# Optimization experiments

Hardware: AMD Instinct MI355X
Metric: run time of the kernel (lower is better)

## Reference

```python
import jax, jax.numpy as jnp
import numpy as np

N = 100000
E = 3200000
G = 2000
EPS = 1e-5

def gcn_conv(x, W, b, src, dst):
    # PyG GCNConv: add self-loops, symmetric deg^-1/2 normalization,
    # out_i = sum_j norm_ij * (x_j @ W) + b
    loop = jnp.arange(N, dtype=src.dtype)
    s = jnp.concatenate([src, loop])
    d = jnp.concatenate([dst, loop])
    deg = jax.ops.segment_sum(jnp.ones_like(d, dtype=x.dtype), d, num_segments=N)
    dinv = jax.lax.rsqrt(jnp.maximum(deg, 1.0))
    norm = dinv[s] * dinv[d]                      # [E+N]
    h = x @ W                                     # [N, out]
    msg = h[s] * norm[:, None]                    # gather + scale
    return jax.ops.segment_sum(msg, d, num_segments=N) + b

def batchnorm(h, g, be):
    mu = jnp.mean(h, axis=0)
    var = jnp.mean((h - mu) ** 2, axis=0)
    return (h - mu) * jax.lax.rsqrt(var + EPS) * g + be

def setup_inputs() -> dict:
    key = jax.random.key(0)
    ks = jax.random.split(key, 16)
    inp = {
        "x": jax.random.normal(ks[0], (N, 10), dtype=jnp.float32),
        "src": jax.random.randint(ks[1], (E,), 0, N, dtype=jnp.int32),
        "dst": jax.random.randint(ks[2], (E,), 0, N, dtype=jnp.int32),
        "batch": jnp.sort(jax.random.randint(ks[3], (N,), 0, G, dtype=jnp.int32)),
        "W1": jax.random.normal(ks[4], (10, 64), dtype=jnp.float32) * 0.3,
        "b1": jnp.zeros((64,), jnp.float32),
        "g1": jnp.ones((64,), jnp.float32),
        "be1": jnp.zeros((64,), jnp.float32),
        "W2": jax.random.normal(ks[5], (64, 128), dtype=jnp.float32) * 0.12,
        "b2": jnp.zeros((128,), jnp.float32),
        "g2": jnp.ones((128,), jnp.float32),
        "be2": jnp.zeros((128,), jnp.float32),
        "fW1": jax.random.normal(ks[6], (128, 64), dtype=jnp.float32) * 0.09,
        "fb1": jnp.zeros((64,), jnp.float32),
        "fW2": jax.random.normal(ks[7], (64, 1), dtype=jnp.float32) * 0.12,
        "fb2": jnp.zeros((1,), jnp.float32),
    }
    return inp

def reference(x, src, dst, batch, W1, b1, g1, be1, W2, b2, g2, be2, fW1, fb1, fW2, fb2):
    h = jax.nn.relu(batchnorm(gcn_conv(x, W1, b1, src, dst), g1, be1))
    h = jax.nn.relu(batchnorm(gcn_conv(h, W2, b2, src, dst), g2, be2))
    # global_mean_pool over graphs
    s = jax.ops.segment_sum(h, batch, num_segments=G)
    cnt = jax.ops.segment_sum(jnp.ones((N,), h.dtype), batch, num_segments=G)
    pooled = s / jnp.maximum(cnt, 1.0)[:, None]   # [G, 128]
    # dropout is identity in eval mode
    h = jax.nn.relu(pooled @ fW1 + fb1)
    return h @ fW2 + fb2                          # [G, 1]
```

## Files before the change

kernel.cpp:

```cpp
#include <hip/hip_runtime.h>
#include <hip/hip_fp16.h>

#define NN 100000
#define NE 3200000
#define NG 2000
#define NB 391
#define BKT_SH 8
#define EPB 4096
#define PAD 16
#define CAP 10240
static constexpr float BN_EPS = 1e-5f;

typedef _Float16 f16x8 __attribute__((ext_vector_type(8)));
typedef float    f32x4 __attribute__((ext_vector_type(4)));

__global__ __launch_bounds__(1024) void k_init(int* bcur, float* s1, float* s2) {
    int t = threadIdx.x;
    if (t < NB) bcur[t * PAD] = t * CAP;
    if (t < 128) s1[t] = 0.f;
    if (t < 256) s2[t] = 0.f;
}

__global__ __launch_bounds__(256) void k_bucket(const int* __restrict__ src, const int* __restrict__ dst,
                                                int* __restrict__ bcur, int* __restrict__ stage) {
    __shared__ int cnt[NB];
    __shared__ int base[NB];
    int t = threadIdx.x;
    long long e0 = (long long)blockIdx.x * EPB;
    int ew[EPB / 256], eb[EPB / 256];
#pragma unroll
    for (int i = 0; i < EPB / 256; ++i) {
        long long e = e0 + t + i * 256;
        if (e < NE) {
            int d = dst[e];
            ew[i] = ((d & 255) << 17) | src[e];
            eb[i] = d >> BKT_SH;
        } else eb[i] = -1;
    }
    for (int i = t; i < NB; i += 256) cnt[i] = 0;
    __syncthreads();
#pragma unroll
    for (int i = 0; i < EPB / 256; ++i)
        if (eb[i] >= 0) atomicAdd(&cnt[eb[i]], 1);
    __syncthreads();
    for (int i = t; i < NB; i += 256) {
        int c = cnt[i];
        base[i] = c ? atomicAdd(&bcur[i * PAD], c) : 0;
    }
    __syncthreads();
    for (int i = t; i < NB; i += 256) cnt[i] = 0;
    __syncthreads();
#pragma unroll
    for (int i = 0; i < EPB / 256; ++i) {
        if (eb[i] >= 0) {
            int pos = base[eb[i]] + atomicAdd(&cnt[eb[i]], 1);
            stage[pos] = ew[i];
        }
    }
}

__global__ __launch_bounds__(256) void k_csr(const int* __restrict__ stage,
                                             const int* __restrict__ bcur, const float* __restrict__ x,
                                             int* __restrict__ deg_i, int* __restrict__ row_start,
                                             float* __restrict__ dinv, int* __restrict__ srcs,
                                             __half2* __restrict__ xh2) {
    __shared__ int ldeg[256];
    __shared__ int scn[256];
    __shared__ int lcur[256];
    int t = threadIdx.x;
    int b = blockIdx.x;
    int base = b * CAP;
    int end  = bcur[b * PAD];
    ldeg[t] = 0;
    __syncthreads();
    for (int e = base + t; e < end; e += 256)
        atomicAdd(&ldeg[(stage[e] >> 17) & 255], 1);
    __syncthreads();
    int v = ldeg[t];
    scn[t] = v;
    __syncthreads();
#pragma unroll
    for (int off = 1; off < 256; off <<= 1) {
        int a = (t >= off) ? scn[t - off] : 0;
        __syncthreads();
        scn[t] += a;
        __syncthreads();
    }
    int rs = base + scn[t] - v;
    lcur[t] = rs;
    int i = (b << BKT_SH) + t;
    if (i < NN) {
        deg_i[i] = v;
        row_start[i] = rs;
        float dv = rsqrtf((float)(v + 1));
        dinv[i] = dv;
        float xv[10];
#pragma unroll
        for (int k = 0; k < 10; ++k) xv[k] = x[i * 10 + k] * dv;
#pragma unroll
        for (int c = 0; c < 8; ++c) {
            float a = (2 * c < 10) ? xv[2 * c] : 0.f;
            float bb = (2 * c + 1 < 10) ? xv[2 * c + 1] : 0.f;
            xh2[i * 8 + c] = __floats2half2_rn(a, bb);
        }
    }
    __syncthreads();
    for (int e = base + t; e < end; e += 256) {
        int w = stage[e];
        int pos = atomicAdd(&lcur[(w >> 17) & 255], 1);
        srcs[pos] = w & 0x1FFFF;
    }
}

__global__ __launch_bounds__(256) void k_gather1(const float4* __restrict__ xh4, const int* __restrict__ srcs,
                                                 const int* __restrict__ row_start, const int* __restrict__ deg,
                                                 const float* __restrict__ dinv, float4* __restrict__ aggx4) {
    int lane = threadIdx.x & 63;
    int wid  = threadIdx.x >> 6;
    int d = blockIdx.x * 4 + wid;
    if (d >= NN) return;
    int c = lane & 1;
    int g = lane >> 1;
    int start = row_start[d];
    int cnt   = deg[d];
    float acc[8] = {0.f};
    for (int k = g; k < cnt; k += 32) {
        int s = srcs[start + k];
        float4 r = xh4[s * 2 + c];
        const __half2* p = (const __half2*)&r;
#pragma unroll
        for (int j = 0; j < 4; ++j) {
            float2 u = __half22float2(p[j]);
            acc[2 * j] += u.x; acc[2 * j + 1] += u.y;
        }
    }
    if (g == 0) {
        float4 r = xh4[d * 2 + c];
        const __half2* p = (const __half2*)&r;
#pragma unroll
        for (int j = 0; j < 4; ++j) {
            float2 u = __half22float2(p[j]);
            acc[2 * j] += u.x; acc[2 * j + 1] += u.y;
        }
    }
#pragma unroll
    for (int m = 2; m < 64; m <<= 1) {
#pragma unroll
        for (int j = 0; j < 8; ++j) acc[j] += __shfl_xor(acc[j], m, 64);
    }
    if (g == 0) {
        float dd = dinv[d];
        float4 o0 = make_float4(dd * acc[0], dd * acc[1], dd * acc[2], dd * acc[3]);
        float4 o1 = make_float4(dd * acc[4], dd * acc[5], dd * acc[6], dd * acc[7]);
        aggx4[d * 4 + c * 2]     = o0;
        aggx4[d * 4 + c * 2 + 1] = o1;
    }
}

__global__ __launch_bounds__(256) void k_mm1s(const float* __restrict__ aggx, const float* __restrict__ W,
                                              const float* __restrict__ b, __half* __restrict__ h1h,
                                              float* __restrict__ sums1) {
    __shared__ float ls[256];
    __shared__ float lq[256];
    int t = threadIdx.x;
    int rg = t >> 6;
    int f = t & 63;
    float w[10];
#pragma unroll
    for (int k = 0; k < 10; ++k) w[k] = W[k * 64 + f];
    float bf = b[f];
    float s = 0.f, q = 0.f;
    for (int row = blockIdx.x * 4 + rg; row < NN; row += 512 * 4) {
        float acc = bf;
#pragma unroll
        for (int k = 0; k < 10; ++k) acc += aggx[row * 16 + k] * w[k];
        s += acc; q += acc * acc;
        h1h[row * 64 + f] = __float2half(acc);
    }
    ls[t] = s; lq[t] = q;
    __syncthreads();
    if (t < 64) {
        float S = ls[t] + ls[t + 64] + ls[t + 128] + ls[t + 192];
        float Q = lq[t] + lq[t + 64] + lq[t + 128] + lq[t + 192];
        atomicAdd(&sums1[f], S);
        atomicAdd(&sums1[64 + f], Q);
    }
}

__global__ __launch_bounds__(256) void k_bn_apply1h(const float4* __restrict__ h1h4, const float* __restrict__ sums1,
                                                    const float* __restrict__ g, const float* __restrict__ be,
                                                    const float* __restrict__ dinv, int2* __restrict__ h1f8) {
    int idx = blockIdx.x * 256 + threadIdx.x;
    if (idx >= NN * 8) return;
    int i = idx >> 3;
    int c = idx & 7;
    const float invn = 1.0f / (float)NN;
    float dv = dinv[i];
    float4 r = h1h4[idx];
    const __half2* p = (const __half2*)&r;
    float rv[8];
#pragma unroll
    for (int j = 0; j < 4; ++j) {
        int f0 = 8 * c + 2 * j, f1 = f0 + 1;
        float mu0 = sums1[f0] * invn, mu1 = sums1[f1] * invn;
        float sc0 = g[f0] * rsqrtf(sums1[64 + f0] * invn - mu0 * mu0 + BN_EPS);
        float sc1 = g[f1] * rsqrtf(sums1[64 + f1] * invn - mu1 * mu1 + BN_EPS);
        float2 u = __half22float2(p[j]);
        rv[2 * j]     = fmaxf((u.x - mu0) * sc0 + be[f0], 0.f) * dv;
        rv[2 * j + 1] = fmaxf((u.y - mu1) * sc1 + be[f1], 0.f) * dv;
    }
    int lo = __builtin_amdgcn_cvt_pk_fp8_f32(rv[0], rv[1], 0, false);
    lo     = __builtin_amdgcn_cvt_pk_fp8_f32(rv[2], rv[3], lo, true);
    int hi = __builtin_amdgcn_cvt_pk_fp8_f32(rv[4], rv[5], 0, false);
    hi     = __builtin_amdgcn_cvt_pk_fp8_f32(rv[6], rv[7], hi, true);
    h1f8[idx] = make_int2(lo, hi);
}

__global__ __launch_bounds__(256) void k_gather2(const int4* __restrict__ h16, const int* __restrict__ srcs,
                                                 const int* __restrict__ row_start, const int* __restrict__ deg,
                                                 const float* __restrict__ dinv, float4* __restrict__ aggh4) {
    int lane = threadIdx.x & 63;
    int wid  = threadIdx.x >> 6;
    int d = blockIdx.x * 4 + wid;
    if (d >= NN) return;
    int c = lane & 3;
    int g = lane >> 2;
    int start = row_start[d];
    int cnt   = deg[d];
    float acc[16];
#pragma unroll
    for (int j = 0; j < 16; ++j) acc[j] = 0.f;
    for (int k = g; k < cnt; k += 16) {
        int s = srcs[start + k];
        int4 w = h16[(long long)s * 4 + c];
#pragma unroll
        for (int j = 0; j < 4; ++j) {
            int wi = (&w.x)[j];
            auto lo = __builtin_amdgcn_cvt_pk_f32_fp8(wi, false);
            auto hi = __builtin_amdgcn_cvt_pk_f32_fp8(wi, true);
            acc[4 * j]     += lo[0]; acc[4 * j + 1] += lo[1];
            acc[4 * j + 2] += hi[0]; acc[4 * j + 3] += hi[1];
        }
    }
    if (g == 0) {
        int4 w = h16[(long long)d * 4 + c];
#pragma unroll
        for (int j = 0; j < 4; ++j) {
            int wi = (&w.x)[j];
            auto lo = __builtin_amdgcn_cvt_pk_f32_fp8(wi, false);
            auto hi = __builtin_amdgcn_cvt_pk_f32_fp8(wi, true);
            acc[4 * j]     += lo[0]; acc[4 * j + 1] += lo[1];
            acc[4 * j + 2] += hi[0]; acc[4 * j + 3] += hi[1];
        }
    }
#pragma unroll
    for (int m = 4; m < 64; m <<= 1) {
#pragma unroll
        for (int j = 0; j < 16; ++j) acc[j] += __shfl_xor(acc[j], m, 64);
    }
    if (g == 0) {
        float dd = dinv[d];
        __half2 o[8];
#pragma unroll
        for (int j = 0; j < 8; ++j)
            o[j] = __floats2half2_rn(dd * acc[2 * j], dd * acc[2 * j + 1]);
        const float4* of = (const float4*)o;
        aggh4[d * 8 + c * 2]     = of[0];
        aggh4[d * 8 + c * 2 + 1] = of[1];
    }
}

__global__ __launch_bounds__(256) void k_mm2m(const __half* __restrict__ aggh, const float* __restrict__ W,
                                              const float* __restrict__ b, __half* __restrict__ h2,
                                              float* __restrict__ sums2) {
    int t = threadIdx.x;
    __shared__ _Float16 w2h[64 * 128];
    for (int i = t; i < 64 * 128; i += 256) w2h[i] = (_Float16)W[i];
    __syncthreads();

    int lane = t & 63;
    int wid  = t >> 6;
    int quad = lane >> 4;
    int n16  = lane & 15;

    f16x8 bfr[8][2];
#pragma unroll
    for (int nt = 0; nt < 8; ++nt)
#pragma unroll
        for (int kk = 0; kk < 2; ++kk)
#pragma unroll
            for (int j = 0; j < 8; ++j)
                bfr[nt][kk][j] = w2h[(kk * 32 + quad * 8 + j) * 128 + nt * 16 + n16];
    float bcol[8];
#pragma unroll
    for (int nt = 0; nt < 8; ++nt) bcol[nt] = b[nt * 16 + n16];

    const f16x8* a8 = (const f16x8*)aggh;
    float s[8] = {0.f}, q[8] = {0.f};

    for (int rt = blockIdx.x * 4 + wid; rt < NN / 16; rt += 256 * 4) {
        int arow = rt * 16 + n16;
        f16x8 a0 = a8[arow * 8 + quad];
        f16x8 a1 = a8[arow * 8 + 4 + quad];
#pragma unroll
        for (int nt = 0; nt < 8; ++nt) {
            f32x4 c = {0.f, 0.f, 0.f, 0.f};
            c = __builtin_amdgcn_mfma_f32_16x16x32_f16(a0, bfr[nt][0], c, 0, 0, 0);
            c = __builtin_amdgcn_mfma_f32_16x16x32_f16(a1, bfr[nt][1], c, 0, 0, 0);
            float bb = bcol[nt];
#pragma unroll
            for (int reg = 0; reg < 4; ++reg) {
                float v = c[reg] + bb;
                s[nt] += v; q[nt] += v * v;
                int row = rt * 16 + quad * 4 + reg;
                h2[(long long)row * 128 + nt * 16 + n16] = __float2half(v);
            }
        }
    }
#pragma unroll
    for (int nt = 0; nt < 8; ++nt) {
        s[nt] += __shfl_xor(s[nt], 16, 64); s[nt] += __shfl_xor(s[nt], 32, 64);
        q[nt] += __shfl_xor(q[nt], 16, 64); q[nt] += __shfl_xor(q[nt], 32, 64);
    }
    __shared__ float lsS[4][128];
    __shared__ float lsQ[4][128];
    if (lane < 16) {
#pragma unroll
        for (int nt = 0; nt < 8; ++nt) {
            lsS[wid][nt * 16 + lane] = s[nt];
            lsQ[wid][nt * 16 + lane] = q[nt];
        }
    }
    __syncthreads();
    if (t < 128) {
        float S = lsS[0][t] + lsS[1][t] + lsS[2][t] + lsS[3][t];
        float Q = lsQ[0][t] + lsQ[1][t] + lsQ[2][t] + lsQ[3][t];
        atomicAdd(&sums2[t], S);
        atomicAdd(&sums2[128 + t], Q);
    }
}

__global__ __launch_bounds__(128) void k_pool(const __half* __restrict__ h2, const float* __restrict__ sums2,
                                              const float* __restrict__ g, const float* __restrict__ be,
                                              const int* __restrict__ batch, float* __restrict__ pooled) {
    int gb = blockIdx.x;
    int f = threadIdx.x;
    int lo = 0, hi = NN;
    while (lo < hi) { int mid = (lo + hi) >> 1; if (batch[mid] < gb) lo = mid + 1; else hi = mid; }
    int start = lo;
    hi = NN;
    while (lo < hi) { int mid = (lo + hi) >> 1; if (batch[mid] < gb + 1) lo = mid + 1; else hi = mid; }
    int end = lo;

    const float invn = 1.0f / (float)NN;
    float mu = sums2[f] * invn;
    float sc = g[f] * rsqrtf(sums2[128 + f] * invn - mu * mu + BN_EPS);
    float bb = be[f];
    float acc = 0.f;
    for (int i = start; i < end; ++i) {
        float v = __half2float(h2[(long long)i * 128 + f]);
        acc += fmaxf((v - mu) * sc + bb, 0.f);
    }
    float inv = 1.0f / fmaxf((float)(end - start), 1.0f);
    pooled[gb * 128 + f] = acc * inv;
}

__global__ __launch_bounds__(64) void k_mlp(const float* __restrict__ pooled,
                                            const float* __restrict__ fW1, const float* __restrict__ fb1,
                                            const float* __restrict__ fW2, const float* __restrict__ fb2,
                                            float* __restrict__ out) {
    int g = blockIdx.x;
    int j = threadIdx.x;
    float acc = fb1[j];
#pragma unroll
    for (int k = 0; k < 128; ++k) acc += pooled[g * 128 + k] * fW1[k * 64 + j];
    float hj = fmaxf(acc, 0.f) * fW2[j];
#pragma unroll
    for (int off = 32; off > 0; off >>= 1) hj += __shfl_down(hj, off, 64);
    if (j == 0) out[g] = hj + fb2[0];
}

extern "C" void kernel_launch(void* const* d_in, const int* in_sizes, int n_in,
                              void* d_out, int out_size, void* d_ws, size_t ws_size,
                              hipStream_t stream) {
    const float* x    = (const float*)d_in[0];
    const int*   src  = (const int*)d_in[1];
    const int*   dst  = (const int*)d_in[2];
    const int*   batch= (const int*)d_in[3];
    const float* W1   = (const float*)d_in[4];
    const float* b1   = (const float*)d_in[5];
    const float* g1   = (const float*)d_in[6];
    const float* be1  = (const float*)d_in[7];
    const float* W2   = (const float*)d_in[8];
    const float* b2   = (const float*)d_in[9];
    const float* g2   = (const float*)d_in[10];
    const float* be2  = (const float*)d_in[11];
    const float* fW1  = (const float*)d_in[12];
    const float* fb1  = (const float*)d_in[13];
    const float* fW2  = (const float*)d_in[14];
    const float* fb2  = (const float*)d_in[15];
    float* out = (float*)d_out;

    float* ws        = (float*)d_ws;
    int*   deg_i     = (int*)ws;
    int*   row_start = deg_i + NN;
    float* dinv      = (float*)(row_start + NN);
    int*   bcur      = (int*)(dinv + NN);
    float* sums1     = (float*)(bcur + NB * PAD);
    float* sums2     = sums1 + 128;
    float* h1R       = sums2 + 256;
    float* agghR     = h1R + NN * 64;
    float* h2R       = agghR + NN * 64;
    __half2* xh2     = (__half2*)h1R;
    __half*  h1h     = (__half*)h1R;
    float*   pooled  = h1R;
    int*     stage   = (int*)agghR;
    __half*  aggh    = (__half*)agghR;
    float*   aggx    = h2R;
    int*     srcs    = (int*)(h2R + NN * 16);
    int2*    h1f8    = (int2*)(h2R + NN * 16 + NB * CAP);
    __half*  h2      = (__half*)h2R;

    k_init<<<1, 1024, 0, stream>>>(bcur, sums1, sums2);
    k_bucket<<<(NE + EPB - 1) / EPB, 256, 0, stream>>>(src, dst, bcur, stage);
    k_csr<<<NB, 256, 0, stream>>>(stage, bcur, x, deg_i, row_start, dinv, srcs, xh2);

    k_gather1<<<(NN + 3) / 4, 256, 0, stream>>>((const float4*)xh2, srcs, row_start, deg_i, dinv, (float4*)aggx);
    k_mm1s<<<512, 256, 0, stream>>>(aggx, W1, b1, h1h, sums1);
    k_bn_apply1h<<<(NN * 8 + 255) / 256, 256, 0, stream>>>((const float4*)h1h, sums1, g1, be1, dinv, h1f8);

    k_gather2<<<(NN + 3) / 4, 256, 0, stream>>>((const int4*)h1f8, srcs, row_start, deg_i, dinv, (float4*)aggh);
    k_mm2m<<<256, 256, 0, stream>>>(aggh, W2, b2, h2, sums2);

    k_pool<<<NG, 128, 0, stream>>>(h2, sums2, g2, be2, batch, pooled);
    k_mlp<<<NG, 64, 0, stream>>>(pooled, fW1, fb1, fW2, fb2, out);
}
```

Measured before the change: 375.8 us.

## Remap gather kernels to lane-per-feature-chunk with multiple nodes per wavefront

Both neighbor-aggregation kernels change from one wavefront per destination node, with lanes split across edges and a cross-lane shuffle reduction, to several nodes per wavefront. Each lane owns a small feature slice and walks that node's whole edge list serially, unrolled by two. This removes the shuffle reductions and the idle lanes left when a node has fewer edges than lane groups, with an average degree of about 32. In exchange, the gather loads per lane are narrower (4 bytes instead of 16) and each lane runs a longer serial dependency chain over edges.

```diff
diff --git a/kernel.cpp b/kernel.cpp
--- a/kernel.cpp
+++ b/kernel.cpp
@@ -112,49 +112,37 @@
     }
 }
 
-__global__ __launch_bounds__(256) void k_gather1(const float4* __restrict__ xh4, const int* __restrict__ srcs,
+__global__ __launch_bounds__(256) void k_gather1(const __half2* __restrict__ xh2, const int* __restrict__ srcs,
                                                  const int* __restrict__ row_start, const int* __restrict__ deg,
-                                                 const float* __restrict__ dinv, float4* __restrict__ aggx4) {
+                                                 const float* __restrict__ dinv, float2* __restrict__ aggx2) {
     int lane = threadIdx.x & 63;
     int wid  = threadIdx.x >> 6;
-    int d = blockIdx.x * 4 + wid;
+    int sub  = lane >> 3;
+    int li   = lane & 7;
+    int d = blockIdx.x * 32 + wid * 8 + sub;
     if (d >= NN) return;
-    int c = lane & 1;
-    int g = lane >> 1;
     int start = row_start[d];
     int cnt   = deg[d];
-    float acc[8] = {0.f};
-    for (int k = g; k < cnt; k += 32) {
+    float ax = 0.f, ay = 0.f;
+    int k = 0;
+    for (; k + 2 <= cnt; k += 2) {
+        int s0 = srcs[start + k];
+        int s1 = srcs[start + k + 1];
+        float2 u0 = __half22float2(xh2[s0 * 8 + li]);
+        float2 u1 = __half22float2(xh2[s1 * 8 + li]);
+        ax += u0.x + u1.x; ay += u0.y + u1.y;
+    }
+    if (k < cnt) {
         int s = srcs[start + k];
-        float4 r = xh4[s * 2 + c];
-        const __half2* p = (const __half2*)&r;
-#pragma unroll
-        for (int j = 0; j < 4; ++j) {
-            float2 u = __half22float2(p[j]);
-            acc[2 * j] += u.x; acc[2 * j + 1] += u.y;
-        }
-    }
-    if (g == 0) {
-        float4 r = xh4[d * 2 + c];
-        const __half2* p = (const __half2*)&r;
-#pragma unroll
-        for (int j = 0; j < 4; ++j) {
-            float2 u = __half22float2(p[j]);
-            acc[2 * j] += u.x; acc[2 * j + 1] += u.y;
-        }
-    }
-#pragma unroll
-    for (int m = 2; m < 64; m <<= 1) {
-#pragma unroll
-        for (int j = 0; j < 8; ++j) acc[j] += __shfl_xor(acc[j], m, 64);
-    }
-    if (g == 0) {
-        float dd = dinv[d];
-        float4 o0 = make_float4(dd * acc[0], dd * acc[1], dd * acc[2], dd * acc[3]);
-        float4 o1 = make_float4(dd * acc[4], dd * acc[5], dd * acc[6], dd * acc[7]);
-        aggx4[d * 4 + c * 2]     = o0;
-        aggx4[d * 4 + c * 2 + 1] = o1;
-    }
+        float2 u = __half22float2(xh2[s * 8 + li]);
+        ax += u.x; ay += u.y;
+    }
+    {
+        float2 u = __half22float2(xh2[d * 8 + li]);
+        ax += u.x; ay += u.y;
+    }
+    float dd = dinv[d];
+    aggx2[d * 8 + li] = make_float2(dd * ax, dd * ay);
 }
 
 __global__ __launch_bounds__(256) void k_mm1s(const float* __restrict__ aggx, const float* __restrict__ W,
@@ -216,58 +204,48 @@
     h1f8[idx] = make_int2(lo, hi);
 }
 
-__global__ __launch_bounds__(256) void k_gather2(const int4* __restrict__ h16, const int* __restrict__ srcs,
+__global__ __launch_bounds__(256) void k_gather2(const int* __restrict__ h1f8i, const int* __restrict__ srcs,
                                                  const int* __restrict__ row_start, const int* __restrict__ deg,
-                                                 const float* __restrict__ dinv, float4* __restrict__ aggh4) {
+                                                 const float* __restrict__ dinv, float2* __restrict__ aggh2) {
     int lane = threadIdx.x & 63;
     int wid  = threadIdx.x >> 6;
-    int d = blockIdx.x * 4 + wid;
+    int sub  = lane >> 4;
+    int li   = lane & 15;
+    int d = blockIdx.x * 16 + wid * 4 + sub;
     if (d >= NN) return;
-    int c = lane & 3;
-    int g = lane >> 2;
     int start = row_start[d];
     int cnt   = deg[d];
-    float acc[16];
-#pragma unroll
-    for (int j = 0; j < 16; ++j) acc[j] = 0.f;
-    for (int k = g; k < cnt; k += 16) {
-        int s = srcs[start + k];
-        int4 w = h16[(long long)s * 4 + c];
-#pragma unroll
-        for (int j = 0; j < 4; ++j) {
-            int wi = (&w.x)[j];
-            auto lo = __builtin_amdgcn_cvt_pk_f32_fp8(wi, false);
-            auto hi = __builtin_amdgcn_cvt_pk_f32_fp8(wi, true);
-            acc[4 * j]     += lo[0]; acc[4 * j + 1] += lo[1];
-            acc[4 * j + 2] += hi[0]; acc[4 * j + 3] += hi[1];
-        }
-    }
-    if (g == 0) {
-        int4 w = h16[(long long)d * 4 + c];
-#pragma unroll
-        for (int j = 0; j < 4; ++j) {
-            int wi = (&w.x)[j];
-            auto lo = __builtin_amdgcn_cvt_pk_f32_fp8(wi, false);
-            auto hi = __builtin_amdgcn_cvt_pk_f32_fp8(wi, true);
-            acc[4 * j]     += lo[0]; acc[4 * j + 1] += lo[1];
-            acc[4 * j + 2] += hi[0]; acc[4 * j + 3] += hi[1];
-        }
-    }
-#pragma unroll
-    for (int m = 4; m < 64; m <<= 1) {
-#pragma unroll
-        for (int j = 0; j < 16; ++j) acc[j] += __shfl_xor(acc[j], m, 64);
-    }
-    if (g == 0) {
-        float dd = dinv[d];
-        __half2 o[8];
-#pragma unroll
-        for (int j = 0; j < 8; ++j)
-            o[j] = __floats2half2_rn(dd * acc[2 * j], dd * acc[2 * j + 1]);
-        const float4* of = (const float4*)o;
-        aggh4[d * 8 + c * 2]     = of[0];
-        aggh4[d * 8 + c * 2 + 1] = of[1];
-    }
+    float a0 = 0.f, a1 = 0.f, a2 = 0.f, a3 = 0.f;
+    int k = 0;
+    for (; k + 2 <= cnt; k += 2) {
+        int s0 = srcs[start + k];
+        int s1 = srcs[start + k + 1];
+        int w0 = h1f8i[s0 * 16 + li];
+        int w1 = h1f8i[s1 * 16 + li];
+        auto l0 = __builtin_amdgcn_cvt_pk_f32_fp8(w0, false);
+        auto h0 = __builtin_amdgcn_cvt_pk_f32_fp8(w0, true);
+        auto l1 = __builtin_amdgcn_cvt_pk_f32_fp8(w1, false);
+        auto h1 = __builtin_amdgcn_cvt_pk_f32_fp8(w1, true);
+        a0 += l0[0] + l1[0]; a1 += l0[1] + l1[1];
+        a2 += h0[0] + h1[0]; a3 += h0[1] + h1[1];
+    }
+    if (k < cnt) {
+        int w = h1f8i[srcs[start + k] * 16 + li];
+        auto lo = __builtin_amdgcn_cvt_pk_f32_fp8(w, false);
+        auto hi = __builtin_amdgcn_cvt_pk_f32_fp8(w, true);
+        a0 += lo[0]; a1 += lo[1]; a2 += hi[0]; a3 += hi[1];
+    }
+    {
+        int w = h1f8i[d * 16 + li];
+        auto lo = __builtin_amdgcn_cvt_pk_f32_fp8(w, false);
+        auto hi = __builtin_amdgcn_cvt_pk_f32_fp8(w, true);
+        a0 += lo[0]; a1 += lo[1]; a2 += hi[0]; a3 += hi[1];
+    }
+    float dd = dinv[d];
+    __half2 o[2];
+    o[0] = __floats2half2_rn(dd * a0, dd * a1);
+    o[1] = __floats2half2_rn(dd * a2, dd * a3);
+    aggh2[d * 16 + li] = *(const float2*)o;
 }
 
 __global__ __launch_bounds__(256) void k_mm2m(const __half* __restrict__ aggh, const float* __restrict__ W,
@@ -425,11 +403,11 @@
     k_bucket<<<(NE + EPB - 1) / EPB, 256, 0, stream>>>(src, dst, bcur, stage);
     k_csr<<<NB, 256, 0, stream>>>(stage, bcur, x, deg_i, row_start, dinv, srcs, xh2);
 
-    k_gather1<<<(NN + 3) / 4, 256, 0, stream>>>((const float4*)xh2, srcs, row_start, deg_i, dinv, (float4*)aggx);
+    k_gather1<<<(NN + 31) / 32, 256, 0, stream>>>(xh2, srcs, row_start, deg_i, dinv, (float2*)aggx);
     k_mm1s<<<512, 256, 0, stream>>>(aggx, W1, b1, h1h, sums1);
     k_bn_apply1h<<<(NN * 8 + 255) / 256, 256, 0, stream>>>((const float4*)h1h, sums1, g1, be1, dinv, h1f8);
 
-    k_gather2<<<(NN + 3) / 4, 256, 0, stream>>>((const int4*)h1f8, srcs, row_start, deg_i, dinv, (float4*)aggh);
+    k_gather2<<<(NN + 15) / 16, 256, 0, stream>>>((const int*)h1f8, srcs, row_start, deg_i, dinv, (float2*)aggh);
     k_mm2m<<<256, 256, 0, stream>>>(aggh, W2, b2, h2, sums2);
 
     k_pool<<<NG, 128, 0, stream>>>(h2, sums2, g2, be2, batch, pooled);
```

Measured after the change: 353.2 us. 6.0% less time.
